# Kernel tuning notes

Measured on AMD Instinct MI355X. Metric: run time of the kernel, lower is better.

The kernel has to match this reference:

```python
import math
import jax, jax.numpy as jnp
import numpy as np

D_MODEL = 1024
N_HEADS = 16
D_K = D_MODEL // N_HEADS
THETA = 10000.0
B, S = 2, 2048


def setup_inputs() -> dict:
    key = jax.random.key(0)
    k1, k2, k3 = jax.random.split(key, 3)
    x = jax.random.normal(k1, (B, S, D_MODEL), dtype=jnp.float32)
    token_positions = jnp.arange(B * S, dtype=jnp.int32).reshape(B, S)
    std_qkv = math.sqrt(2.0 / (D_MODEL + 3 * D_MODEL))
    std_o = math.sqrt(2.0 / (D_MODEL + D_MODEL))
    W_qkv = jax.random.truncated_normal(k2, -3.0, 3.0, (3 * D_MODEL, D_MODEL), dtype=jnp.float32) * std_qkv
    W_o = jax.random.truncated_normal(k3, -3.0, 3.0, (D_MODEL, D_MODEL), dtype=jnp.float32) * std_o
    return {"x": x, "W_qkv": W_qkv, "W_o": W_o, "token_positions": token_positions}


def _rope(x, pos):
    # x: (B, H, S, D_K); pos: (B, S) int
    half = D_K // 2
    inv_freq = 1.0 / (THETA ** (jnp.arange(0, D_K, 2, dtype=jnp.float32) / D_K))  # (half,)
    # pos_extended = pos[:, None, :] -> freqs (B, 1, S, half)
    freqs = pos[:, None, :, None].astype(jnp.float32) * inv_freq
    cos, sin = jnp.cos(freqs), jnp.sin(freqs)
    xr = x.reshape(*x.shape[:-1], half, 2)
    x1, x2 = xr[..., 0], xr[..., 1]
    out = jnp.stack([x1 * cos - x2 * sin, x2 * cos + x1 * sin], axis=-1)
    return out.reshape(x.shape)


def reference(x, W_qkv, W_o, token_positions):
    seq_len = x.shape[-2]
    qkv = jnp.einsum('bsi,oi->bso', x, W_qkv)
    q, k, v = jnp.split(qkv, 3, axis=-1)
    # (B, S, H*D) -> (B, H, S, D)
    def to_heads(t):
        return t.reshape(t.shape[0], t.shape[1], N_HEADS, D_K).transpose(0, 2, 1, 3)
    q, k, v = to_heads(q), to_heads(k), to_heads(v)
    q = _rope(q, token_positions)
    k = _rope(k, token_positions)
    scores = jnp.einsum('bhnd,bhmd->bhnm', q, k) / math.sqrt(D_K)
    causal = jnp.tril(jnp.ones((seq_len, seq_len), dtype=bool))
    scores = jnp.where(causal, scores, -jnp.inf)
    attn = jax.nn.softmax(scores, axis=-1)
    out = jnp.einsum('bhnm,bhmd->bhnd', attn, v)
    out = out.transpose(0, 2, 1, 3).reshape(x.shape[0], seq_len, D_MODEL)
    return jnp.einsum('bsi,oi->bso', out, W_o)
```

## Files before the change

### kernel.cpp

```cpp
#include <hip/hip_runtime.h>
#include <cmath>

typedef __bf16 bf16;
typedef bf16 bf16x4 __attribute__((ext_vector_type(4)));
typedef bf16 bf16x8 __attribute__((ext_vector_type(8)));
typedef float f32x4 __attribute__((ext_vector_type(4)));

#define MFMA16(a, b, c) __builtin_amdgcn_mfma_f32_16x16x32_bf16(a, b, c, 0, 0, 0)

__global__ __launch_bounds__(256) void cvt_all(
    const float* __restrict__ x, const float* __restrict__ wqkv,
    const float* __restrict__ wo, bf16* __restrict__ xb,
    bf16* __restrict__ wqkvb, bf16* __restrict__ wob) {
  int i = (blockIdx.x * 256 + threadIdx.x) * 4;
  const float* src;
  bf16* dst;
  if (i < (4 << 20)) {
    src = x + i; dst = xb + i;
  } else if (i < (7 << 20)) {
    src = wqkv + (i - (4 << 20)); dst = wqkvb + (i - (4 << 20));
  } else {
    src = wo + (i - (7 << 20)); dst = wob + (i - (7 << 20));
  }
  const f32x4 v = *(const f32x4*)src;
  bf16x4 o = {(bf16)v[0], (bf16)v[1], (bf16)v[2], (bf16)v[3]};
  *(bf16x4*)dst = o;
}

template <int EPI>
__global__ __launch_bounds__(256) void gemm_nt(
    const bf16* __restrict__ A, const bf16* __restrict__ Bm,
    const int* __restrict__ tokpos,
    bf16* __restrict__ out0, bf16* __restrict__ out1, bf16* __restrict__ out2,
    float* __restrict__ outF, int N) {
  __shared__ __align__(16) bf16 As[2][128 * 32];
  __shared__ __align__(16) bf16 Bs[2][128 * 32];
  const int tid = threadIdx.x;
  const int w = tid >> 6, lane = tid & 63, quad = lane >> 4, m16 = lane & 15;
  const int m0 = blockIdx.y * 128, n0 = blockIdx.x * 128;
  const int wm = (w >> 1) * 64, wn = (w & 1) * 64;

  f32x4 acc[4][4] = {};

  const int row0 = tid >> 2, ch = tid & 3;
  const bf16* Ag0 = A + (size_t)(m0 + row0) * 1024 + ch * 8;
  const bf16* Ag1 = A + (size_t)(m0 + 64 + row0) * 1024 + ch * 8;
  const bf16* Bg0 = Bm + (size_t)(n0 + row0) * 1024 + ch * 8;
  const bf16* Bg1 = Bm + (size_t)(n0 + 64 + row0) * 1024 + ch * 8;

  bf16x8 ra0, ra1, rb0, rb1;
  auto LOAD = [&](int k0) {
    ra0 = *(const bf16x8*)(Ag0 + k0);
    ra1 = *(const bf16x8*)(Ag1 + k0);
    rb0 = *(const bf16x8*)(Bg0 + k0);
    rb1 = *(const bf16x8*)(Bg1 + k0);
  };
  auto WRITE = [&](int p) {
    *(bf16x8*)(As[p] + tid * 8) = ra0;
    *(bf16x8*)(As[p] + 2048 + tid * 8) = ra1;
    *(bf16x8*)(Bs[p] + tid * 8) = rb0;
    *(bf16x8*)(Bs[p] + 2048 + tid * 8) = rb1;
  };

  LOAD(0);
  WRITE(0);
  __syncthreads();

  int p = 0;
  for (int k0 = 0; k0 < 1024; k0 += 32) {
    const bool more = (k0 + 32) < 1024;
    if (more) LOAD(k0 + 32);
    bf16x8 af[4], bfr[4];
#pragma unroll
    for (int mi = 0; mi < 4; ++mi)
      af[mi] = *(const bf16x8*)(As[p] + (wm + mi * 16 + m16) * 32 + quad * 8);
#pragma unroll
    for (int ni = 0; ni < 4; ++ni)
      bfr[ni] = *(const bf16x8*)(Bs[p] + (wn + ni * 16 + m16) * 32 + quad * 8);
#pragma unroll
    for (int mi = 0; mi < 4; ++mi)
#pragma unroll
      for (int ni = 0; ni < 4; ++ni)
        acc[mi][ni] = MFMA16(af[mi], bfr[ni], acc[mi][ni]);
    if (more) {
      WRITE(1 - p);
      __syncthreads();
      p ^= 1;
    }
  }

  if constexpr (EPI == 0) {
#pragma unroll
    for (int mi = 0; mi < 4; ++mi) {
      int rowb = m0 + wm + mi * 16 + quad * 4;
#pragma unroll
      for (int r = 0; r < 4; ++r) {
        size_t off = (size_t)(rowb + r) * N + n0 + wn;
#pragma unroll
        for (int ni = 0; ni < 4; ++ni)
          outF[off + ni * 16 + m16] = acc[mi][ni][r];
      }
    }
  } else {
#pragma unroll
    for (int mi = 0; mi < 4; ++mi) {
      int rowb = m0 + wm + mi * 16 + quad * 4;
      int pos4[4];
#pragma unroll
      for (int r = 0; r < 4; ++r) pos4[r] = tokpos[rowb + r];
#pragma unroll
      for (int ni = 0; ni < 4; ++ni) {
        int col = n0 + wn + ni * 16 + m16;
        int sec = col >> 10, f = col & 1023, h = f >> 6, d = f & 63;
        if (sec == 2) {
#pragma unroll
          for (int r = 0; r < 4; ++r) {
            int row = rowb + r;
            int bb = row >> 11, s = row & 2047;
            out2[((size_t)(bb * 16 + h) * 64 + d) * 2048 + s] =
                (bf16)acc[mi][ni][r];
          }
        } else {
          float inv = __expf(-(float)(d & ~1) * (9.2103403719762f / 64.f));
          bf16* dst = sec ? out1 : out0;
          const float sc = sec ? 1.0f : 0.125f;
#pragma unroll
          for (int r = 0; r < 4; ++r) {
            float v = acc[mi][ni][r];
            float vp = __shfl_xor(v, 1);
            float ang = (float)pos4[r] * inv;
            float cs, sn;
            __sincosf(ang, &sn, &cs);
            float ov = (d & 1) ? (v * cs + vp * sn) : (v * cs - vp * sn);
            ov *= sc;
            int row = rowb + r;
            int bb = row >> 11, s = row & 2047;
            dst[((size_t)(bb * 16 + h) * 2048 + s) * 64 + d] = (bf16)ov;
          }
        }
      }
    }
  }
}

__global__ __launch_bounds__(256) void attn_kernel(
    const bf16* __restrict__ Q, const bf16* __restrict__ K,
    const bf16* __restrict__ Vt, bf16* __restrict__ O) {
  __shared__ __align__(16) bf16 KP[3][64 * 72];
  __shared__ __align__(16) bf16 VP[3][64 * 72];
  __shared__ __align__(16) bf16 PS[4][16 * 72];
  const int tid = threadIdx.x;
  const int w = tid >> 6, lane = tid & 63, quad = lane >> 4, m16 = lane & 15;
  const int bh = blockIdx.x;
  const int j = blockIdx.y;
  const int qtA = j, qtB = 31 - j;
  const int q0A = qtA * 64, q0B = qtB * 64;
  const bf16* Qb = Q + (size_t)bh * 2048 * 64;
  const bf16* Kb = K + (size_t)bh * 2048 * 64;
  const bf16* Vb = Vt + (size_t)bh * 64 * 2048;

  const int ch0 = w * 8, ch1 = (w + 4) * 8;
  const bf16* Kg = Kb + (size_t)lane * 64;
  const bf16* Vg = Vb + (size_t)lane * 2048;

  const bf16* qrowA = Qb + (size_t)(q0A + w * 16 + m16) * 64;
  const bf16* qrowB = Qb + (size_t)(q0B + w * 16 + m16) * 64;
  bf16x8 aqA[2], aqB[2];
  aqA[0] = *(const bf16x8*)(qrowA + quad * 8);
  aqA[1] = *(const bf16x8*)(qrowA + 32 + quad * 8);
  aqB[0] = *(const bf16x8*)(qrowB + quad * 8);
  aqB[1] = *(const bf16x8*)(qrowB + 32 + quad * 8);

  bf16x8 rk0, rk1, rv0, rv1;
  auto PREFETCH = [&](int kt) {
    rk0 = *(const bf16x8*)(Kg + (size_t)kt * 64 * 64 + ch0);
    rk1 = *(const bf16x8*)(Kg + (size_t)kt * 64 * 64 + ch1);
    rv0 = *(const bf16x8*)(Vg + kt * 64 + ch0);
    rv1 = *(const bf16x8*)(Vg + kt * 64 + ch1);
  };
  auto STAGE = [&](int p) {
    *(bf16x8*)(KP[p] + lane * 72 + ch0) = rk0;
    *(bf16x8*)(KP[p] + lane * 72 + ch1) = rk1;
    *(bf16x8*)(VP[p] + lane * 72 + ch0) = rv0;
    *(bf16x8*)(VP[p] + lane * 72 + ch1) = rv1;
  };

  PREFETCH(0);
  STAGE(0);
  PREFETCH(1);
  STAGE(1);
  __syncthreads();

  auto QK = [&](int p, const bf16x8* aq, f32x4* sa) {
#pragma unroll
    for (int kk = 0; kk < 2; ++kk)
#pragma unroll
      for (int ni = 0; ni < 4; ++ni) {
        bf16x8 bk = *(const bf16x8*)(KP[p] + (ni * 16 + m16) * 72 + kk * 32 +
                                     quad * 8);
        sa[ni] = MFMA16(aq[kk], bk, sa[ni]);
      }
  };

  f32x4 oA[4] = {}, oB[4] = {};
  float lA[4] = {0.f, 0.f, 0.f, 0.f}, lB[4] = {0.f, 0.f, 0.f, 0.f};
  const int qrel = w * 16 + quad * 4;

  auto SOFTPV = [&](int p, const f32x4* sa, f32x4* o, float* lp, bool diag) {
    bf16* ps = PS[w];
#pragma unroll
    for (int r = 0; r < 4; ++r) {
#pragma unroll
      for (int ni = 0; ni < 4; ++ni) {
        float pp = exp2f(fmaf(sa[ni][r], 1.44269504f, -11.5415603f));
        if (diag && (ni * 16 + m16) > qrel + r) pp = 0.f;
        lp[r] += pp;
        ps[(quad * 4 + r) * 72 + ni * 16 + m16] = (bf16)pp;
      }
    }
    bf16x8 ap[2];
    ap[0] = *(const bf16x8*)(ps + m16 * 72 + quad * 8);
    ap[1] = *(const bf16x8*)(ps + m16 * 72 + 32 + quad * 8);
#pragma unroll
    for (int kk = 0; kk < 2; ++kk)
#pragma unroll
      for (int ng = 0; ng < 4; ++ng) {
        bf16x8 bv = *(const bf16x8*)(VP[p] + (ng * 16 + m16) * 72 + kk * 32 +
                                     quad * 8);
        o[ng] = MFMA16(ap[kk], bv, o[ng]);
      }
  };

  f32x4 saA[4] = {}, saB[4] = {};
  QK(0, aqB, saB);
  QK(0, aqA, saA);

  int pc = 0, pn = 1, pst = 2;
  for (int kt = 0; kt <= qtB; ++kt) {
    const bool more = kt < qtB;
    const bool stage2 = (kt + 2) <= qtB;
    if (stage2) PREFETCH(kt + 2);

    f32x4 saBn[4] = {}, saAn[4] = {};
    if (more) QK(pn, aqB, saBn);
    if (kt + 1 <= qtA) QK(pn, aqA, saAn);

    SOFTPV(pc, saB, oB, lB, kt == qtB);
    if (kt <= qtA) SOFTPV(pc, saA, oA, lA, kt == qtA);

    if (stage2) STAGE(pst);
    if (more) __syncthreads();

#pragma unroll
    for (int i = 0; i < 4; ++i) { saB[i] = saBn[i]; saA[i] = saAn[i]; }
    int t = pc; pc = pn; pn = pst; pst = t;
  }

  const int b = bh >> 4, h = bh & 15;
  auto epilogue = [&](f32x4* o, float* lp, int q0) {
#pragma unroll
    for (int r = 0; r < 4; ++r) {
      float l = lp[r];
      l += __shfl_xor(l, 1);
      l += __shfl_xor(l, 2);
      l += __shfl_xor(l, 4);
      l += __shfl_xor(l, 8);
      float inv_l = 1.f / l;
      int s = q0 + w * 16 + quad * 4 + r;
      size_t rowoff = (size_t)(b * 2048 + s) * 1024 + h * 64;
#pragma unroll
      for (int ng = 0; ng < 4; ++ng)
        O[rowoff + ng * 16 + m16] = (bf16)(o[ng][r] * inv_l);
    }
  };
  epilogue(oA, lA, q0A);
  epilogue(oB, lB, q0B);
}

extern "C" void kernel_launch(void* const* d_in, const int* in_sizes, int n_in,
                              void* d_out, int out_size, void* d_ws, size_t ws_size,
                              hipStream_t stream) {
  (void)in_sizes; (void)n_in; (void)out_size; (void)ws_size;
  const float* x = (const float*)d_in[0];
  const float* Wqkv = (const float*)d_in[1];
  const float* Wo = (const float*)d_in[2];
  const int* tokpos = (const int*)d_in[3];
  float* out = (float*)d_out;

  const size_t NEL = (size_t)2 * 16 * 2048 * 64;
  bf16* Qws = (bf16*)d_ws;
  bf16* Kws = Qws + NEL;
  bf16* Vtw = Kws + NEL;
  bf16* Ows = Vtw + NEL;
  bf16* xb  = Ows + NEL;
  bf16* Wqkvb = xb + NEL;
  bf16* Wob = Wqkvb + (size_t)3072 * 1024;

  cvt_all<<<8192, 256, 0, stream>>>(x, Wqkv, Wo, xb, Wqkvb, Wob);

  gemm_nt<1><<<dim3(24, 32), 256, 0, stream>>>(xb, Wqkvb, tokpos, Qws, Kws,
                                               Vtw, nullptr, 3072);
  attn_kernel<<<dim3(32, 16), 256, 0, stream>>>(Qws, Kws, Vtw, Ows);
  gemm_nt<0><<<dim3(8, 32), 256, 0, stream>>>(Ows, Wob, nullptr, nullptr,
                                              nullptr, nullptr, out, 1024);
}
```

Baseline: 198.5 us.

## Load K/V MFMA fragments directly from global memory, dropping LDS staging

The attention kernel stops staging K and V tiles through triple-buffered shared memory with register prefetch and block barriers. Each wave now loads its K and V MFMA operand fragments straight from global memory every iteration and computes QK^T without a software pipeline. This removes LDS traffic and __syncthreads. The cost is that all four waves now redundantly read the same K/V data from global or cache, and the loads are no longer prefetched ahead of the math, so memory latency is exposed.

```diff
diff --git a/kernel.cpp b/kernel.cpp
--- a/kernel.cpp
+++ b/kernel.cpp
@@ -146,8 +146,6 @@
 __global__ __launch_bounds__(256) void attn_kernel(
     const bf16* __restrict__ Q, const bf16* __restrict__ K,
     const bf16* __restrict__ Vt, bf16* __restrict__ O) {
-  __shared__ __align__(16) bf16 KP[3][64 * 72];
-  __shared__ __align__(16) bf16 VP[3][64 * 72];
   __shared__ __align__(16) bf16 PS[4][16 * 72];
   const int tid = threadIdx.x;
   const int w = tid >> 6, lane = tid & 63, quad = lane >> 4, m16 = lane & 15;
@@ -156,12 +154,9 @@
   const int qtA = j, qtB = 31 - j;
   const int q0A = qtA * 64, q0B = qtB * 64;
   const bf16* Qb = Q + (size_t)bh * 2048 * 64;
-  const bf16* Kb = K + (size_t)bh * 2048 * 64;
-  const bf16* Vb = Vt + (size_t)bh * 64 * 2048;
-
-  const int ch0 = w * 8, ch1 = (w + 4) * 8;
-  const bf16* Kg = Kb + (size_t)lane * 64;
-  const bf16* Vg = Vb + (size_t)lane * 2048;
+
+  const bf16* Kfrag = K + (size_t)bh * 2048 * 64 + m16 * 64 + quad * 8;
+  const bf16* Vfrag = Vt + (size_t)bh * 64 * 2048 + m16 * 2048 + quad * 8;
 
   const bf16* qrowA = Qb + (size_t)(q0A + w * 16 + m16) * 64;
   const bf16* qrowB = Qb + (size_t)(q0B + w * 16 + m16) * 64;
@@ -171,42 +166,12 @@
   aqB[0] = *(const bf16x8*)(qrowB + quad * 8);
   aqB[1] = *(const bf16x8*)(qrowB + 32 + quad * 8);
 
-  bf16x8 rk0, rk1, rv0, rv1;
-  auto PREFETCH = [&](int kt) {
-    rk0 = *(const bf16x8*)(Kg + (size_t)kt * 64 * 64 + ch0);
-    rk1 = *(const bf16x8*)(Kg + (size_t)kt * 64 * 64 + ch1);
-    rv0 = *(const bf16x8*)(Vg + kt * 64 + ch0);
-    rv1 = *(const bf16x8*)(Vg + kt * 64 + ch1);
-  };
-  auto STAGE = [&](int p) {
-    *(bf16x8*)(KP[p] + lane * 72 + ch0) = rk0;
-    *(bf16x8*)(KP[p] + lane * 72 + ch1) = rk1;
-    *(bf16x8*)(VP[p] + lane * 72 + ch0) = rv0;
-    *(bf16x8*)(VP[p] + lane * 72 + ch1) = rv1;
-  };
-
-  PREFETCH(0);
-  STAGE(0);
-  PREFETCH(1);
-  STAGE(1);
-  __syncthreads();
-
-  auto QK = [&](int p, const bf16x8* aq, f32x4* sa) {
-#pragma unroll
-    for (int kk = 0; kk < 2; ++kk)
-#pragma unroll
-      for (int ni = 0; ni < 4; ++ni) {
-        bf16x8 bk = *(const bf16x8*)(KP[p] + (ni * 16 + m16) * 72 + kk * 32 +
-                                     quad * 8);
-        sa[ni] = MFMA16(aq[kk], bk, sa[ni]);
-      }
-  };
-
   f32x4 oA[4] = {}, oB[4] = {};
   float lA[4] = {0.f, 0.f, 0.f, 0.f}, lB[4] = {0.f, 0.f, 0.f, 0.f};
   const int qrel = w * 16 + quad * 4;
 
-  auto SOFTPV = [&](int p, const f32x4* sa, f32x4* o, float* lp, bool diag) {
+  auto SOFTPV = [&](const bf16x8 (&bv)[2][4], const f32x4* sa, f32x4* o,
+                    float* lp, bool diag) {
     bf16* ps = PS[w];
 #pragma unroll
     for (int r = 0; r < 4; ++r) {
@@ -224,36 +189,37 @@
 #pragma unroll
     for (int kk = 0; kk < 2; ++kk)
 #pragma unroll
-      for (int ng = 0; ng < 4; ++ng) {
-        bf16x8 bv = *(const bf16x8*)(VP[p] + (ng * 16 + m16) * 72 + kk * 32 +
-                                     quad * 8);
-        o[ng] = MFMA16(ap[kk], bv, o[ng]);
-      }
-  };
-
-  f32x4 saA[4] = {}, saB[4] = {};
-  QK(0, aqB, saB);
-  QK(0, aqA, saA);
-
-  int pc = 0, pn = 1, pst = 2;
+      for (int ng = 0; ng < 4; ++ng)
+        o[ng] = MFMA16(ap[kk], bv[kk][ng], o[ng]);
+  };
+
   for (int kt = 0; kt <= qtB; ++kt) {
-    const bool more = kt < qtB;
-    const bool stage2 = (kt + 2) <= qtB;
-    if (stage2) PREFETCH(kt + 2);
-
-    f32x4 saBn[4] = {}, saAn[4] = {};
-    if (more) QK(pn, aqB, saBn);
-    if (kt + 1 <= qtA) QK(pn, aqA, saAn);
-
-    SOFTPV(pc, saB, oB, lB, kt == qtB);
-    if (kt <= qtA) SOFTPV(pc, saA, oA, lA, kt == qtA);
-
-    if (stage2) STAGE(pst);
-    if (more) __syncthreads();
-
-#pragma unroll
-    for (int i = 0; i < 4; ++i) { saB[i] = saBn[i]; saA[i] = saAn[i]; }
-    int t = pc; pc = pn; pn = pst; pst = t;
+    bf16x8 bk[2][4], bv[2][4];
+#pragma unroll
+    for (int kk = 0; kk < 2; ++kk)
+#pragma unroll
+      for (int ni = 0; ni < 4; ++ni) {
+        bk[kk][ni] =
+            *(const bf16x8*)(Kfrag + ((size_t)kt * 64 + ni * 16) * 64 + kk * 32);
+        bv[kk][ni] =
+            *(const bf16x8*)(Vfrag + (size_t)ni * 16 * 2048 + kt * 64 + kk * 32);
+      }
+    const bool haveA = kt <= qtA;
+    f32x4 saB[4] = {}, saA[4] = {};
+#pragma unroll
+    for (int kk = 0; kk < 2; ++kk)
+#pragma unroll
+      for (int ni = 0; ni < 4; ++ni)
+        saB[ni] = MFMA16(aqB[kk], bk[kk][ni], saB[ni]);
+    if (haveA) {
+#pragma unroll
+      for (int kk = 0; kk < 2; ++kk)
+#pragma unroll
+        for (int ni = 0; ni < 4; ++ni)
+          saA[ni] = MFMA16(aqA[kk], bk[kk][ni], saA[ni]);
+    }
+    SOFTPV(bv, saB, oB, lB, kt == qtB);
+    if (haveA) SOFTPV(bv, saA, oA, lA, kt == qtA);
   }
 
   const int b = bh >> 4, h = bh & 15;
```

Measured after the change: 249.0 us. +25.4%, slower.
